# Performance work log

Measured on AMD Instinct MI355X. Metric: run time of the kernel, lower is better.

## Reference

```python
import jax, jax.numpy as jnp
import numpy as np

EMBED_DIM = 1024
NUM_HEADS = 16
HEAD_DIM = EMBED_DIM // NUM_HEADS
SCALE = HEAD_DIM ** -0.5


def setup_inputs() -> dict:
    key = jax.random.key(0)
    ks = jax.random.split(key, 12)
    B, S, D = 4, 2048, EMBED_DIM
    x = jax.random.normal(ks[0], (B, S, D), dtype=jnp.float32)
    key_padding_mask = jax.random.randint(ks[1], (B, S), 0, 2).astype(jnp.bool_)
    init = 1.0 / np.sqrt(D)
    def lin(kw, kb):
        W = jax.random.uniform(kw, (D, D), minval=-init, maxval=init, dtype=jnp.float32)
        b = jax.random.uniform(kb, (D,), minval=-init, maxval=init, dtype=jnp.float32)
        return W, b
    Wq, bq = lin(ks[2], ks[3])
    Wk, bk = lin(ks[4], ks[5])
    Wv, bv = lin(ks[6], ks[7])
    Wo, bo = lin(ks[8], ks[9])
    return {"x": x, "key_padding_mask": key_padding_mask,
            "Wq": Wq, "bq": bq, "Wk": Wk, "bk": bk,
            "Wv": Wv, "bv": bv, "Wo": Wo, "bo": bo}


def reference(x, key_padding_mask, Wq, bq, Wk, bk, Wv, bv, Wo, bo):
    B, S, D = x.shape
    H, Hd = NUM_HEADS, HEAD_DIM
    # projections (torch Linear: y = x @ W.T + b)
    q = (x @ Wq.T + bq).reshape(B, S, H, Hd).transpose(0, 2, 1, 3)  # [B,H,S,Hd]
    k = (x @ Wk.T + bk).reshape(B, S, H, Hd).transpose(0, 2, 1, 3)
    v = (x @ Wv.T + bv).reshape(B, S, H, Hd).transpose(0, 2, 1, 3)
    scores = jnp.einsum('bhqd,bhkd->bhqk', q, k) * SCALE  # [B,H,S,S]
    mask = key_padding_mask[:, None, None, :]  # [B,1,1,S]
    scores = jnp.where(mask, -jnp.inf, scores)
    probs = jax.nn.softmax(scores, axis=-1)
    # dropout p=0.0 (inference) -> identity
    out = jnp.einsum('bhqk,bhkd->bhqd', probs, v)  # [B,H,S,Hd]
    out = out.transpose(0, 2, 1, 3).reshape(B, S, D)
    return out @ Wo.T + bo
```

## Files before the change

### kernel.cpp

```cpp
#include <hip/hip_runtime.h>
#include <stdint.h>

typedef __bf16 bf16;
typedef __bf16 bf16x8 __attribute__((ext_vector_type(8)));
typedef float f32x4 __attribute__((ext_vector_type(4)));

#define SEQ 2048
#define NHEAD 16
#define HDIM 64
#define DMODEL 1024
#define NBATCH 4
#define ATT_SCALE 0.18033688011112042f
#define SEQHD (SEQ * HDIM)
#define BHSTRIDE (2 * SEQHD)


__device__ __forceinline__ void gload_lds16(const bf16* g, bf16* l) {
  __builtin_amdgcn_global_load_lds(
      (const __attribute__((address_space(1))) uint32_t*)g,
      (__attribute__((address_space(3))) uint32_t*)l, 16, 0, 0);
}

__device__ __forceinline__ uint32_t pk2(float a, float b) {
  bf16 x = (bf16)a, y = (bf16)b;
  return (uint32_t)__builtin_bit_cast(uint16_t, x) |
         ((uint32_t)__builtin_bit_cast(uint16_t, y) << 16);
}

__global__ __launch_bounds__(256) void cvt_kernel(const float* __restrict__ src,
                                                  bf16* __restrict__ dst) {
  size_t i = ((size_t)blockIdx.x * 256 + threadIdx.x) * 16;
#pragma unroll
  for (int j = 0; j < 2; ++j) {
    float4 f0 = *(const float4*)(src + i + j * 8);
    float4 f1 = *(const float4*)(src + i + j * 8 + 4);
    bf16x8 v;
    v[0] = (bf16)f0.x; v[1] = (bf16)f0.y; v[2] = (bf16)f0.z; v[3] = (bf16)f0.w;
    v[4] = (bf16)f1.x; v[5] = (bf16)f1.y; v[6] = (bf16)f1.z; v[7] = (bf16)f1.w;
    *(bf16x8*)(dst + i + j * 8) = v;
  }
}

__global__ __launch_bounds__(256) void prep_kernel(
    const float* __restrict__ Wq, const float* __restrict__ Wk,
    const float* __restrict__ Wv, bf16* __restrict__ Wbf3,
    int* __restrict__ posv, int* __restrict__ inv) {
  __shared__ int sums[256];
  const int bx = blockIdx.x, t = threadIdx.x;
  if (bx < 768) {
    const float* s = bx < 256 ? Wq : (bx < 512 ? Wk : Wv);
    bf16* d = Wbf3 + (size_t)(bx >> 8) * DMODEL * DMODEL;
    size_t i = ((size_t)(bx & 255) * 256 + t) * 16;
#pragma unroll
    for (int j = 0; j < 2; ++j) {
      float4 f0 = *(const float4*)(s + i + j * 8);
      float4 f1 = *(const float4*)(s + i + j * 8 + 4);
      bf16x8 v;
      v[0] = (bf16)f0.x; v[1] = (bf16)f0.y; v[2] = (bf16)f0.z; v[3] = (bf16)f0.w;
      v[4] = (bf16)f1.x; v[5] = (bf16)f1.y; v[6] = (bf16)f1.z; v[7] = (bf16)f1.w;
      *(bf16x8*)(d + i + j * 8) = v;
    }
    return;
  }
  const int b = bx - 768;
  int* m = posv + b * SEQ;
  int* iv = inv + b * SEQ;
  int f[8], cnt = 0;
#pragma unroll
  for (int j = 0; j < 8; ++j) {
    int x = m[t * 8 + j];
    int unm = (x < 0) ? 0 : ((x & 0x40000000) ? 1 : (x == 0 ? 1 : 0));
    f[j] = unm; cnt += unm;
    iv[t * 8 + j] = 0;
  }
  sums[t] = cnt;
  __syncthreads();
  if (t == 0) {
    int acc = 0;
#pragma unroll 8
    for (int i = 0; i < 256; ++i) { int s = sums[i]; sums[i] = acc; acc += s; }
  }
  __syncthreads();
  int p = sums[t];
#pragma unroll
  for (int j = 0; j < 8; ++j) {
    m[t * 8 + j] = (int)((f[j] ? 0x40000000u : 0x80000000u) | (unsigned)p);
    if (f[j]) iv[p] = t * 8 + j;
    p += f[j];
  }
}

__global__ __launch_bounds__(256) void mega_kernel(
    const bf16* __restrict__ xb, const bf16* __restrict__ Wall,
    const float* __restrict__ bq, const float* __restrict__ bk,
    const float* __restrict__ bv, const int* __restrict__ posv,
    const int* __restrict__ inv, bf16* __restrict__ Qall,
    bf16* __restrict__ kv, const float* __restrict__ Wo,
    bf16* __restrict__ Wobf) {
  __shared__ __align__(16) bf16 lW[64 * 64];
  __shared__ __align__(16) bf16 lXw[4][32 * 64];
  const int bx = blockIdx.x;
  const int t = threadIdx.x, wave = t >> 6, lane = t & 63;
  const int quad = lane >> 4, c = lane & 15;
  const int sr = lane >> 3, sg = lane & 7;
  const int swzc = (sg ^ sr) * 8;

  if (bx >= 2048) {
    size_t i = ((size_t)(bx - 2048) * 256 + t) * 16;
#pragma unroll
    for (int j = 0; j < 2; ++j) {
      float4 f0 = *(const float4*)(Wo + i + j * 8);
      float4 f1 = *(const float4*)(Wo + i + j * 8 + 4);
      bf16x8 v;
      v[0] = (bf16)f0.x; v[1] = (bf16)f0.y; v[2] = (bf16)f0.z; v[3] = (bf16)f0.w;
      v[4] = (bf16)f1.x; v[5] = (bf16)f1.y; v[6] = (bf16)f1.z; v[7] = (bf16)f1.w;
      *(bf16x8*)(Wobf + i + j * 8) = v;
    }
    return;
  }

  if (bx < 1024) {
    const int m0 = (bx & 63) * 128;
    const int h = bx >> 6;
    const bf16* W = Wall + (size_t)(h * HDIM) * DMODEL;
    bf16* pw = lXw[wave];
    const bf16* aS = xb + (size_t)(m0 + wave * 32 + sr) * DMODEL + swzc;
    const bf16* wS = W + (size_t)(wave * 8 + sr) * DMODEL + swzc;
    f32x4 acc[2][4] = {};
    for (int k0 = 0; k0 < DMODEL; k0 += 64) {
      __syncthreads();
      gload_lds16(wS + k0, lW + wave * 512);
      gload_lds16(wS + 32 * DMODEL + k0, lW + wave * 512 + 2048);
#pragma unroll
      for (int ii = 0; ii < 4; ++ii)
        gload_lds16(aS + k0 + (size_t)ii * 8 * DMODEL, pw + ii * 512);
      __syncthreads();
#pragma unroll
      for (int kk = 0; kk < 2; ++kk) {
        bf16x8 af[2], bfr[4];
#pragma unroll
        for (int mi = 0; mi < 2; ++mi) {
          int row = mi * 16 + c;
          af[mi] = *(const bf16x8*)(pw + row * 64 + (((kk * 4 + quad) ^ (row & 7)) * 8));
        }
#pragma unroll
        for (int ni = 0; ni < 4; ++ni) {
          int row = ni * 16 + c;
          bfr[ni] = *(const bf16x8*)(lW + row * 64 + (((kk * 4 + quad) ^ (row & 7)) * 8));
        }
#pragma unroll
        for (int mi = 0; mi < 2; ++mi)
#pragma unroll
          for (int ni = 0; ni < 4; ++ni)
            acc[mi][ni] = __builtin_amdgcn_mfma_f32_16x16x32_bf16(af[mi], bfr[ni], acc[mi][ni], 0, 0, 0);
      }
    }
#pragma unroll
    for (int ni = 0; ni < 4; ++ni) {
      int hd = ni * 16 + c;
      float bqv = bq[h * HDIM + hd];
#pragma unroll
      for (int mi = 0; mi < 2; ++mi)
#pragma unroll
        for (int r = 0; r < 4; ++r) {
          int tok = m0 + wave * 32 + mi * 16 + quad * 4 + r;
          int b = tok >> 11, s = tok & 2047;
          Qall[((size_t)(b * NHEAD + h) * SEQ + s) * HDIM + hd] =
              (bf16)((acc[mi][ni][r] + bqv) * ATT_SCALE);
        }
    }
    return;
  }

  const int idx = bx - 1024;
  const int xi = idx & 31, yi = idx >> 5;
  const int b_loc = xi >> 4, mb = xi & 15;
  const int isV = yi >> 4, h = yi & 15;
  int v2 = posv[b_loc * SEQ + SEQ - 1];
  int nk = (v2 & 0x3FFFFFFF) + (v2 >= 0 ? 1 : 0);
  const int c0 = mb * 128;
  if (c0 >= nk) return;
  const bf16* W = Wall + (size_t)(1 + isV) * DMODEL * DMODEL + (size_t)(h * HDIM) * DMODEL;
  const float* bias = (isV ? bv : bk) + h * HDIM;
  bf16* pw = lXw[wave];
  const bf16* wS = W + (size_t)(wave * 8 + sr) * DMODEL + swzc;
  const int* invb = inv + b_loc * SEQ;
  int grow[4];
#pragma unroll
  for (int ii = 0; ii < 4; ++ii)
    grow[ii] = invb[c0 + wave * 32 + ii * 8 + sr];
  const bf16* xbb = xb + (size_t)b_loc * SEQ * DMODEL + swzc;
  f32x4 acc[2][4] = {};
  for (int k0 = 0; k0 < DMODEL; k0 += 64) {
    __syncthreads();
    gload_lds16(wS + k0, lW + wave * 512);
    gload_lds16(wS + 32 * DMODEL + k0, lW + wave * 512 + 2048);
#pragma unroll
    for (int ii = 0; ii < 4; ++ii)
      gload_lds16(xbb + (size_t)grow[ii] * DMODEL + k0, pw + ii * 512);
    __syncthreads();
#pragma unroll
    for (int kk = 0; kk < 2; ++kk) {
      bf16x8 af[2], bfr[4];
#pragma unroll
      for (int mi = 0; mi < 2; ++mi) {
        int row = mi * 16 + c;
        af[mi] = *(const bf16x8*)(pw + row * 64 + (((kk * 4 + quad) ^ (row & 7)) * 8));
      }
#pragma unroll
      for (int ni = 0; ni < 4; ++ni) {
        int row = ni * 16 + c;
        bfr[ni] = *(const bf16x8*)(lW + row * 64 + (((kk * 4 + quad) ^ (row & 7)) * 8));
      }
#pragma unroll
      for (int mi = 0; mi < 2; ++mi)
#pragma unroll
        for (int ni = 0; ni < 4; ++ni)
          acc[mi][ni] = __builtin_amdgcn_mfma_f32_16x16x32_bf16(af[mi], bfr[ni], acc[mi][ni], 0, 0, 0);
    }
  }
  bf16* base = kv + (size_t)(b_loc * NHEAD + h) * BHSTRIDE;
#pragma unroll
  for (int ni = 0; ni < 4; ++ni) {
    int hd = ni * 16 + c;
    float bv_ = bias[hd];
#pragma unroll
    for (int mi = 0; mi < 2; ++mi)
#pragma unroll
      for (int r = 0; r < 4; ++r) {
        int dst = c0 + wave * 32 + mi * 16 + quad * 4 + r;
        float val = (dst < nk) ? (acc[mi][ni][r] + bv_) : 0.0f;
        if (isV) base[SEQHD + (size_t)hd * SEQ + dst] = (bf16)val;
        else     base[(size_t)dst * HDIM + hd] = (bf16)val;
      }
  }
}

__global__ __launch_bounds__(256) void kvproj_kernel(
    const bf16* __restrict__ xb, const bf16* __restrict__ Wall,
    const float* __restrict__ bk, const float* __restrict__ bv,
    const int* __restrict__ posv, const int* __restrict__ inv,
    bf16* __restrict__ kv) {
  __shared__ __align__(16) bf16 lW[64 * 64];
  __shared__ __align__(16) bf16 lXw[4][32 * 64];
  const int t = threadIdx.x, wave = t >> 6, lane = t & 63;
  const int quad = lane >> 4, c = lane & 15;
  const int bx = blockIdx.x;
  const int b_loc = bx >> 4, mb = bx & 15;
  const int nt = blockIdx.y;
  const int isV = nt >> 4, h = nt & 15;
  int v2 = posv[b_loc * SEQ + SEQ - 1];
  int nk = (v2 & 0x3FFFFFFF) + (v2 >= 0 ? 1 : 0);
  const int c0 = mb * 128;
  if (c0 >= nk) return;
  const bf16* W = Wall + (size_t)(1 + isV) * DMODEL * DMODEL + (size_t)(h * HDIM) * DMODEL;
  const float* bias = (isV ? bv : bk) + h * HDIM;
  bf16* pw = lXw[wave];
  const int sr = lane >> 3, sg = lane & 7;
  const int swzc = (sg ^ sr) * 8;
  const bf16* wS = W + (size_t)(wave * 8 + sr) * DMODEL + swzc;
  const int* invb = inv + b_loc * SEQ;
  int grow[4];
#pragma unroll
  for (int ii = 0; ii < 4; ++ii)
    grow[ii] = invb[c0 + wave * 32 + ii * 8 + sr];
  const bf16* xbb = xb + (size_t)b_loc * SEQ * DMODEL + swzc;
  f32x4 acc[2][4] = {};
  for (int k0 = 0; k0 < DMODEL; k0 += 64) {
    __syncthreads();
    gload_lds16(wS + k0, lW + wave * 512);
    gload_lds16(wS + 32 * DMODEL + k0, lW + wave * 512 + 2048);
#pragma unroll
    for (int ii = 0; ii < 4; ++ii)
      gload_lds16(xbb + (size_t)grow[ii] * DMODEL + k0, pw + ii * 512);
    __syncthreads();
#pragma unroll
    for (int kk = 0; kk < 2; ++kk) {
      bf16x8 af[2], bfr[4];
#pragma unroll
      for (int mi = 0; mi < 2; ++mi) {
        int row = mi * 16 + c;
        af[mi] = *(const bf16x8*)(pw + row * 64 + (((kk * 4 + quad) ^ (row & 7)) * 8));
      }
#pragma unroll
      for (int ni = 0; ni < 4; ++ni) {
        int row = ni * 16 + c;
        bfr[ni] = *(const bf16x8*)(lW + row * 64 + (((kk * 4 + quad) ^ (row & 7)) * 8));
      }
#pragma unroll
      for (int mi = 0; mi < 2; ++mi)
#pragma unroll
        for (int ni = 0; ni < 4; ++ni)
          acc[mi][ni] = __builtin_amdgcn_mfma_f32_16x16x32_bf16(af[mi], bfr[ni], acc[mi][ni], 0, 0, 0);
    }
  }
  bf16* base = kv + (size_t)(b_loc * NHEAD + h) * BHSTRIDE;
#pragma unroll
  for (int ni = 0; ni < 4; ++ni) {
    int hd = ni * 16 + c;
    float bv_ = bias[hd];
#pragma unroll
    for (int mi = 0; mi < 2; ++mi)
#pragma unroll
      for (int r = 0; r < 4; ++r) {
        int dst = c0 + wave * 32 + mi * 16 + quad * 4 + r;
        float val = (dst < nk) ? (acc[mi][ni][r] + bv_) : 0.0f;
        if (isV) base[SEQHD + (size_t)hd * SEQ + dst] = (bf16)val;
        else     base[(size_t)dst * HDIM + hd] = (bf16)val;
      }
  }
}

__global__ __launch_bounds__(256, 4) void attn4_kernel(
    const bf16* __restrict__ Qall, const bf16* __restrict__ KV,
    const int* __restrict__ posv, bf16* __restrict__ O, int chunk) {
  __shared__ __align__(16) bf16 lK[2][64 * 64];
  __shared__ __align__(16) bf16 lV[2][64 * 64];
  __shared__ __align__(16) bf16 lPw[4][16 * 64];
  const int t = threadIdx.x, wave = t >> 6, lane = t & 63;
  const int quad = lane >> 4, c = lane & 15;
  const int i = blockIdx.x;
  const int xcd = i & 7, slot = i >> 3;
  const int bhl = xcd * 4 + (slot >> 5);
  const int qt = slot & 31;
  const int b_loc = bhl >> 4, h = bhl & 15;
  const int b = chunk * 2 + b_loc;
  const int q0 = qt * 64 + wave * 16;
  const bf16* Qh = Qall + (size_t)(b * NHEAD + h) * SEQHD;
  const bf16* Kb = KV + (size_t)(b_loc * NHEAD + h) * BHSTRIDE;
  const bf16* Vtb = Kb + SEQHD;
  bf16* pw = lPw[wave];

  int v2 = posv[b * SEQ + SEQ - 1];
  int nk = (v2 & 0x3FFFFFFF) + (v2 >= 0 ? 1 : 0);
  int NT = ((nk + 63) >> 6) << 6;

  const int srow = t >> 3;
  const int sswz = (t & 7) ^ (srow & 7);
  const bf16* kSrc = Kb + (size_t)srow * HDIM + sswz * 8;
  const bf16* vSrc = Vtb + (size_t)srow * SEQ + sswz * 8;
  const int sOff = wave * 512;

  bf16x8 qf[2];
#pragma unroll
  for (int kk = 0; kk < 2; ++kk)
    qf[kk] = *(const bf16x8*)(Qh + (size_t)(q0 + c) * HDIM + kk * 32 + quad * 8);

  f32x4 oacc[4] = {};
  float mrun = -1e30f, lrun = 0.0f;

  const int pbase = c * 64 + (quad & 1) * 4;
  const int pswz = c & 7;

#pragma unroll
  for (int i2 = 0; i2 < 2; ++i2) {
    gload_lds16(kSrc + i2 * 32 * HDIM, &lK[0][0] + sOff + i2 * 2048);
    gload_lds16(vSrc + (size_t)i2 * 32 * SEQ, &lV[0][0] + sOff + i2 * 2048);
  }
  __syncthreads();

  int idx = 0;
  for (int kt = 0; kt < NT; kt += 64, idx ^= 1) {
    if (kt + 64 < NT) {
      const bf16* ks = kSrc + (size_t)(kt + 64) * HDIM;
      const bf16* vs = vSrc + (kt + 64);
      bf16* kD = &lK[0][0] + (idx ^ 1) * 4096 + sOff;
      bf16* vD = &lV[0][0] + (idx ^ 1) * 4096 + sOff;
#pragma unroll
      for (int i2 = 0; i2 < 2; ++i2) {
        gload_lds16(ks + i2 * 32 * HDIM, kD + i2 * 2048);
        gload_lds16(vs + (size_t)i2 * 32 * SEQ, vD + i2 * 2048);
      }
    }
    const bf16* lKc = &lK[0][0] + idx * 4096;
    const bf16* lVc = &lV[0][0] + idx * 4096;

    f32x4 sacc[4] = {};
    __builtin_amdgcn_s_setprio(1);
#pragma unroll
    for (int kk = 0; kk < 2; ++kk) {
      bf16x8 kf[4];
#pragma unroll
      for (int ni = 0; ni < 4; ++ni) {
        int row = ni * 16 + c;
        kf[ni] = *(const bf16x8*)(lKc + row * 64 + (((kk * 4 + quad) ^ (row & 7)) * 8));
      }
#pragma unroll
      for (int ni = 0; ni < 4; ++ni)
        sacc[ni] = __builtin_amdgcn_mfma_f32_16x16x32_bf16(kf[ni], qf[kk], sacc[ni], 0, 0, 0);
    }
    __builtin_amdgcn_s_setprio(0);

    if (kt + 64 > nk) {
      int base = kt + quad * 4 - nk;
#pragma unroll
      for (int ni = 0; ni < 4; ++ni)
#pragma unroll
        for (int r = 0; r < 4; ++r)
          if (base + ni * 16 + r >= 0) sacc[ni][r] = -3e38f;
    }

    float m1 = fmaxf(fmaxf(sacc[0][0], sacc[0][1]), sacc[0][2]);
    float m2 = fmaxf(fmaxf(sacc[0][3], sacc[1][0]), sacc[1][1]);
    float m3 = fmaxf(fmaxf(sacc[1][2], sacc[1][3]), sacc[2][0]);
    float m4 = fmaxf(fmaxf(sacc[2][1], sacc[2][2]), sacc[2][3]);
    float m5 = fmaxf(fmaxf(sacc[3][0], sacc[3][1]), sacc[3][2]);
    float mx = fmaxf(fmaxf(fmaxf(m1, m2), m3), fmaxf(fmaxf(m4, m5), sacc[3][3]));
    mx = fmaxf(mx, __shfl_xor(mx, 16));
    mx = fmaxf(mx, __shfl_xor(mx, 32));

    if (!__all(mx - mrun <= 8.0f)) {
      float mn = fmaxf(mrun, mx);
      float al = __builtin_amdgcn_exp2f(mrun - mn);
      mrun = mn;
      lrun *= al;
      float al4[4];
#pragma unroll
      for (int r = 0; r < 4; ++r) al4[r] = __shfl(al, quad * 4 + r);
#pragma unroll
      for (int ni = 0; ni < 4; ++ni)
#pragma unroll
        for (int r = 0; r < 4; ++r) oacc[ni][r] *= al4[r];
    }

    float rs = 0.0f;
#pragma unroll
    for (int ni = 0; ni < 4; ++ni)
#pragma unroll
      for (int r = 0; r < 4; ++r) {
        float e = __builtin_amdgcn_exp2f(sacc[ni][r] - mrun);
        sacc[ni][r] = e; rs += e;
      }
    rs += __shfl_xor(rs, 16);
    rs += __shfl_xor(rs, 32);
    lrun += rs;

#pragma unroll
    for (int ni = 0; ni < 4; ++ni) {
      uint2 u;
      u.x = pk2(sacc[ni][0], sacc[ni][1]);
      u.y = pk2(sacc[ni][2], sacc[ni][3]);
      int sl = pbase + (((ni * 2 + (quad >> 1)) ^ pswz) * 8);
      *(uint2*)(pw + sl) = u;
    }

    __builtin_amdgcn_s_setprio(1);
#pragma unroll
    for (int kk = 0; kk < 2; ++kk) {
      bf16x8 pf, vfr[4];
      pf = *(const bf16x8*)(pw + c * 64 + (((kk * 4 + quad) ^ (c & 7)) * 8));
#pragma unroll
      for (int ni = 0; ni < 4; ++ni) {
        int row = ni * 16 + c;
        vfr[ni] = *(const bf16x8*)(lVc + row * 64 + (((kk * 4 + quad) ^ (row & 7)) * 8));
      }
#pragma unroll
      for (int ni = 0; ni < 4; ++ni)
        oacc[ni] = __builtin_amdgcn_mfma_f32_16x16x32_bf16(pf, vfr[ni], oacc[ni], 0, 0, 0);
    }
    __builtin_amdgcn_s_setprio(0);

    __syncthreads();
  }

  float linv = lrun > 0.0f ? 1.0f / lrun : 0.0f;
  float linv4[4];
#pragma unroll
  for (int r = 0; r < 4; ++r) linv4[r] = __shfl(linv, quad * 4 + r);
#pragma unroll
  for (int r = 0; r < 4; ++r) {
    size_t tok = (size_t)b * SEQ + q0 + quad * 4 + r;
#pragma unroll
    for (int ni = 0; ni < 4; ++ni)
      O[tok * DMODEL + h * HDIM + ni * 16 + c] = (bf16)(oacc[ni][r] * linv4[r]);
  }
}

__global__ __launch_bounds__(256) void outproj_kernel(
    const bf16* __restrict__ O, const bf16* __restrict__ Wob,
    const float* __restrict__ bo, float* __restrict__ out) {
  __shared__ __align__(16) bf16 lW[64 * 64];
  __shared__ __align__(16) bf16 lXw[4][32 * 64];
  const int t = threadIdx.x, wave = t >> 6, lane = t & 63;
  const int quad = lane >> 4, c = lane & 15;
  const int m0 = blockIdx.x * 128;
  const int n0 = blockIdx.y * 64;
  bf16* pw = lXw[wave];
  const int sr = lane >> 3, sg = lane & 7;
  const bf16* aS = O + (size_t)(m0 + wave * 32 + sr) * DMODEL + ((sg ^ sr) * 8);
  const bf16* wS = Wob + (size_t)(n0 + wave * 8 + sr) * DMODEL + ((sg ^ sr) * 8);
  f32x4 acc[2][4] = {};
  for (int k0 = 0; k0 < DMODEL; k0 += 64) {
    __syncthreads();
    gload_lds16(wS + k0, lW + wave * 512);
    gload_lds16(wS + 32 * DMODEL + k0, lW + wave * 512 + 2048);
#pragma unroll
    for (int ii = 0; ii < 4; ++ii)
      gload_lds16(aS + k0 + (size_t)ii * 8 * DMODEL, pw + ii * 512);
    __syncthreads();
#pragma unroll
    for (int kk = 0; kk < 2; ++kk) {
      bf16x8 af[2], bfr[4];
#pragma unroll
      for (int mi = 0; mi < 2; ++mi) {
        int row = mi * 16 + c;
        af[mi] = *(const bf16x8*)(pw + row * 64 + (((kk * 4 + quad) ^ (row & 7)) * 8));
      }
#pragma unroll
      for (int ni = 0; ni < 4; ++ni) {
        int row = ni * 16 + c;
        bfr[ni] = *(const bf16x8*)(lW + row * 64 + (((kk * 4 + quad) ^ (row & 7)) * 8));
      }
#pragma unroll
      for (int mi = 0; mi < 2; ++mi)
#pragma unroll
        for (int ni = 0; ni < 4; ++ni)
          acc[mi][ni] = __builtin_amdgcn_mfma_f32_16x16x32_bf16(af[mi], bfr[ni], acc[mi][ni], 0, 0, 0);
    }
  }
#pragma unroll
  for (int ni = 0; ni < 4; ++ni) {
    int gn = n0 + ni * 16 + c;
    float bv_ = bo[gn];
#pragma unroll
    for (int mi = 0; mi < 2; ++mi)
#pragma unroll
      for (int r = 0; r < 4; ++r) {
        int gm = m0 + wave * 32 + mi * 16 + quad * 4 + r;
        out[(size_t)gm * DMODEL + gn] = acc[mi][ni][r] + bv_;
      }
  }
}

extern "C" void kernel_launch(void* const* d_in, const int* in_sizes, int n_in,
                              void* d_out, int out_size, void* d_ws, size_t ws_size,
                              hipStream_t stream) {
  const float* x  = (const float*)d_in[0];
  int*         posv = (int*)d_in[1];
  const float* Wq = (const float*)d_in[2]; const float* bq = (const float*)d_in[3];
  const float* Wk = (const float*)d_in[4]; const float* bk = (const float*)d_in[5];
  const float* Wv = (const float*)d_in[6]; const float* bv = (const float*)d_in[7];
  const float* Wo = (const float*)d_in[8]; const float* bo = (const float*)d_in[9];
  float* out = (float*)d_out;
  char* outc = (char*)d_out;
  char* xc   = (char*)d_in[0];
  const size_t half = (size_t)NBATCH * SEQ * DMODEL * 2;
  const size_t qtr  = half / 2;

  bf16* Qall = (bf16*)d_out;
  bf16* xbf  = (bf16*)(outc + half);
  bf16* KV   = (bf16*)xc;
  bf16* O    = (bf16*)(xc + half);
  bf16* Wbf3 = (bf16*)(xc + half + qtr);
  int*  inv  = (int*)(xc + half + qtr + (size_t)3 * DMODEL * DMODEL * 2);
  bf16* Wobf = (bf16*)d_in[2];

  cvt_kernel<<<dim3(2048), 256, 0, stream>>>(x, xbf);
  prep_kernel<<<dim3(772), 256, 0, stream>>>(Wq, Wk, Wv, Wbf3, posv, inv);
  mega_kernel<<<dim3(2304), 256, 0, stream>>>(xbf, Wbf3, bq, bk, bv, posv, inv,
                                              Qall, KV, Wo, Wobf);
  attn4_kernel<<<dim3(1024), 256, 0, stream>>>(Qall, KV, posv, O, 0);
  kvproj_kernel<<<dim3(32, 32), 256, 0, stream>>>(xbf + (size_t)2 * SEQ * DMODEL, Wbf3, bk, bv,
                                                  posv + 2 * SEQ, inv + 2 * SEQ, KV);
  attn4_kernel<<<dim3(1024), 256, 0, stream>>>(Qall, KV, posv, O, 1);
  outproj_kernel<<<dim3(64, 16), 256, 0, stream>>>(O, Wobf, bo, out);
}
```

Measured before the change: 274.9 us.

## Double-buffer LDS tiles in projection GEMMs to overlap loads with MFMA

Doubles the LDS staging buffers in the Q/K/V projection paths and the output projection, and restructures the K loop so the next 64-wide K slice is issued via global_load_lds while the current slice is consumed by MFMAs. This halves the barriers per K step and aims to hide global-memory latency behind compute. LDS use per block doubles (32KB), which may lower occupancy. The correctness of the direct-to-LDS async loads relies on the barrier draining outstanding loads.

New measurement: 305.6 us. 1.11x slower.

```diff
diff --git a/kernel.cpp b/kernel.cpp
--- a/kernel.cpp
+++ b/kernel.cpp
@@ -97,8 +97,8 @@
     const int* __restrict__ inv, bf16* __restrict__ Qall,
     bf16* __restrict__ kv, const float* __restrict__ Wo,
     bf16* __restrict__ Wobf) {
-  __shared__ __align__(16) bf16 lW[64 * 64];
-  __shared__ __align__(16) bf16 lXw[4][32 * 64];
+  __shared__ __align__(16) bf16 lW[2][64 * 64];
+  __shared__ __align__(16) bf16 lXw[2][4][32 * 64];
   const int bx = blockIdx.x;
   const int t = threadIdx.x, wave = t >> 6, lane = t & 63;
   const int quad = lane >> 4, c = lane & 15;
@@ -123,30 +123,30 @@
     const int m0 = (bx & 63) * 128;
     const int h = bx >> 6;
     const bf16* W = Wall + (size_t)(h * HDIM) * DMODEL;
-    bf16* pw = lXw[wave];
     const bf16* aS = xb + (size_t)(m0 + wave * 32 + sr) * DMODEL + swzc;
     const bf16* wS = W + (size_t)(wave * 8 + sr) * DMODEL + swzc;
     f32x4 acc[2][4] = {};
-    for (int k0 = 0; k0 < DMODEL; k0 += 64) {
-      __syncthreads();
-      gload_lds16(wS + k0, lW + wave * 512);
-      gload_lds16(wS + 32 * DMODEL + k0, lW + wave * 512 + 2048);
+
+    auto stage = [&](int k0, bf16* lWd, bf16* pwd) {
+      gload_lds16(wS + k0, lWd + wave * 512);
+      gload_lds16(wS + 32 * DMODEL + k0, lWd + wave * 512 + 2048);
 #pragma unroll
       for (int ii = 0; ii < 4; ++ii)
-        gload_lds16(aS + k0 + (size_t)ii * 8 * DMODEL, pw + ii * 512);
-      __syncthreads();
+        gload_lds16(aS + k0 + (size_t)ii * 8 * DMODEL, pwd + ii * 512);
+    };
+    auto compute = [&](const bf16* lWc, const bf16* pwc) {
 #pragma unroll
       for (int kk = 0; kk < 2; ++kk) {
         bf16x8 af[2], bfr[4];
 #pragma unroll
         for (int mi = 0; mi < 2; ++mi) {
           int row = mi * 16 + c;
-          af[mi] = *(const bf16x8*)(pw + row * 64 + (((kk * 4 + quad) ^ (row & 7)) * 8));
+          af[mi] = *(const bf16x8*)(pwc + row * 64 + (((kk * 4 + quad) ^ (row & 7)) * 8));
         }
 #pragma unroll
         for (int ni = 0; ni < 4; ++ni) {
           int row = ni * 16 + c;
-          bfr[ni] = *(const bf16x8*)(lW + row * 64 + (((kk * 4 + quad) ^ (row & 7)) * 8));
+          bfr[ni] = *(const bf16x8*)(lWc + row * 64 + (((kk * 4 + quad) ^ (row & 7)) * 8));
         }
 #pragma unroll
         for (int mi = 0; mi < 2; ++mi)
@@ -154,6 +154,17 @@
           for (int ni = 0; ni < 4; ++ni)
             acc[mi][ni] = __builtin_amdgcn_mfma_f32_16x16x32_bf16(af[mi], bfr[ni], acc[mi][ni], 0, 0, 0);
       }
+    };
+
+    stage(0, lW[0], lXw[0][wave]);
+    __syncthreads();
+    for (int k0 = 0; k0 < DMODEL; k0 += 128) {
+      stage(k0 + 64, lW[1], lXw[1][wave]);
+      compute(lW[0], lXw[0][wave]);
+      __syncthreads();
+      if (k0 + 128 < DMODEL) stage(k0 + 128, lW[0], lXw[0][wave]);
+      compute(lW[1], lXw[1][wave]);
+      __syncthreads();
     }
 #pragma unroll
     for (int ni = 0; ni < 4; ++ni) {
@@ -182,7 +193,6 @@
   if (c0 >= nk) return;
   const bf16* W = Wall + (size_t)(1 + isV) * DMODEL * DMODEL + (size_t)(h * HDIM) * DMODEL;
   const float* bias = (isV ? bv : bk) + h * HDIM;
-  bf16* pw = lXw[wave];
   const bf16* wS = W + (size_t)(wave * 8 + sr) * DMODEL + swzc;
   const int* invb = inv + b_loc * SEQ;
   int grow[4];
@@ -191,26 +201,27 @@
     grow[ii] = invb[c0 + wave * 32 + ii * 8 + sr];
   const bf16* xbb = xb + (size_t)b_loc * SEQ * DMODEL + swzc;
   f32x4 acc[2][4] = {};
-  for (int k0 = 0; k0 < DMODEL; k0 += 64) {
-    __syncthreads();
-    gload_lds16(wS + k0, lW + wave * 512);
-    gload_lds16(wS + 32 * DMODEL + k0, lW + wave * 512 + 2048);
+
+  auto stage = [&](int k0, bf16* lWd, bf16* pwd) {
+    gload_lds16(wS + k0, lWd + wave * 512);
+    gload_lds16(wS + 32 * DMODEL + k0, lWd + wave * 512 + 2048);
 #pragma unroll
     for (int ii = 0; ii < 4; ++ii)
-      gload_lds16(xbb + (size_t)grow[ii] * DMODEL + k0, pw + ii * 512);
-    __syncthreads();
+      gload_lds16(xbb + (size_t)grow[ii] * DMODEL + k0, pwd + ii * 512);
+  };
+  auto compute = [&](const bf16* lWc, const bf16* pwc) {
 #pragma unroll
     for (int kk = 0; kk < 2; ++kk) {
       bf16x8 af[2], bfr[4];
 #pragma unroll
       for (int mi = 0; mi < 2; ++mi) {
         int row = mi * 16 + c;
-        af[mi] = *(const bf16x8*)(pw + row * 64 + (((kk * 4 + quad) ^ (row & 7)) * 8));
+        af[mi] = *(const bf16x8*)(pwc + row * 64 + (((kk * 4 + quad) ^ (row & 7)) * 8));
       }
 #pragma unroll
       for (int ni = 0; ni < 4; ++ni) {
         int row = ni * 16 + c;
-        bfr[ni] = *(const bf16x8*)(lW + row * 64 + (((kk * 4 + quad) ^ (row & 7)) * 8));
+        bfr[ni] = *(const bf16x8*)(lWc + row * 64 + (((kk * 4 + quad) ^ (row & 7)) * 8));
       }
 #pragma unroll
       for (int mi = 0; mi < 2; ++mi)
@@ -218,6 +229,17 @@
         for (int ni = 0; ni < 4; ++ni)
           acc[mi][ni] = __builtin_amdgcn_mfma_f32_16x16x32_bf16(af[mi], bfr[ni], acc[mi][ni], 0, 0, 0);
     }
+  };
+
+  stage(0, lW[0], lXw[0][wave]);
+  __syncthreads();
+  for (int k0 = 0; k0 < DMODEL; k0 += 128) {
+    stage(k0 + 64, lW[1], lXw[1][wave]);
+    compute(lW[0], lXw[0][wave]);
+    __syncthreads();
+    if (k0 + 128 < DMODEL) stage(k0 + 128, lW[0], lXw[0][wave]);
+    compute(lW[1], lXw[1][wave]);
+    __syncthreads();
   }
   bf16* base = kv + (size_t)(b_loc * NHEAD + h) * BHSTRIDE;
 #pragma unroll
@@ -241,8 +263,8 @@
     const float* __restrict__ bk, const float* __restrict__ bv,
     const int* __restrict__ posv, const int* __restrict__ inv,
     bf16* __restrict__ kv) {
-  __shared__ __align__(16) bf16 lW[64 * 64];
-  __shared__ __align__(16) bf16 lXw[4][32 * 64];
+  __shared__ __align__(16) bf16 lW[2][64 * 64];
+  __shared__ __align__(16) bf16 lXw[2][4][32 * 64];
   const int t = threadIdx.x, wave = t >> 6, lane = t & 63;
   const int quad = lane >> 4, c = lane & 15;
   const int bx = blockIdx.x;
@@ -255,7 +277,6 @@
   if (c0 >= nk) return;
   const bf16* W = Wall + (size_t)(1 + isV) * DMODEL * DMODEL + (size_t)(h * HDIM) * DMODEL;
   const float* bias = (isV ? bv : bk) + h * HDIM;
-  bf16* pw = lXw[wave];
   const int sr = lane >> 3, sg = lane & 7;
   const int swzc = (sg ^ sr) * 8;
   const bf16* wS = W + (size_t)(wave * 8 + sr) * DMODEL + swzc;
@@ -266,26 +287,27 @@
     grow[ii] = invb[c0 + wave * 32 + ii * 8 + sr];
   const bf16* xbb = xb + (size_t)b_loc * SEQ * DMODEL + swzc;
   f32x4 acc[2][4] = {};
-  for (int k0 = 0; k0 < DMODEL; k0 += 64) {
-    __syncthreads();
-    gload_lds16(wS + k0, lW + wave * 512);
-    gload_lds16(wS + 32 * DMODEL + k0, lW + wave * 512 + 2048);
+
+  auto stage = [&](int k0, bf16* lWd, bf16* pwd) {
+    gload_lds16(wS + k0, lWd + wave * 512);
+    gload_lds16(wS + 32 * DMODEL + k0, lWd + wave * 512 + 2048);
 #pragma unroll
     for (int ii = 0; ii < 4; ++ii)
-      gload_lds16(xbb + (size_t)grow[ii] * DMODEL + k0, pw + ii * 512);
-    __syncthreads();
+      gload_lds16(xbb + (size_t)grow[ii] * DMODEL + k0, pwd + ii * 512);
+  };
+  auto compute = [&](const bf16* lWc, const bf16* pwc) {
 #pragma unroll
     for (int kk = 0; kk < 2; ++kk) {
       bf16x8 af[2], bfr[4];
 #pragma unroll
       for (int mi = 0; mi < 2; ++mi) {
         int row = mi * 16 + c;
-        af[mi] = *(const bf16x8*)(pw + row * 64 + (((kk * 4 + quad) ^ (row & 7)) * 8));
+        af[mi] = *(const bf16x8*)(pwc + row * 64 + (((kk * 4 + quad) ^ (row & 7)) * 8));
       }
 #pragma unroll
       for (int ni = 0; ni < 4; ++ni) {
         int row = ni * 16 + c;
-        bfr[ni] = *(const bf16x8*)(lW + row * 64 + (((kk * 4 + quad) ^ (row & 7)) * 8));
+        bfr[ni] = *(const bf16x8*)(lWc + row * 64 + (((kk * 4 + quad) ^ (row & 7)) * 8));
       }
 #pragma unroll
       for (int mi = 0; mi < 2; ++mi)
@@ -293,6 +315,17 @@
         for (int ni = 0; ni < 4; ++ni)
           acc[mi][ni] = __builtin_amdgcn_mfma_f32_16x16x32_bf16(af[mi], bfr[ni], acc[mi][ni], 0, 0, 0);
     }
+  };
+
+  stage(0, lW[0], lXw[0][wave]);
+  __syncthreads();
+  for (int k0 = 0; k0 < DMODEL; k0 += 128) {
+    stage(k0 + 64, lW[1], lXw[1][wave]);
+    compute(lW[0], lXw[0][wave]);
+    __syncthreads();
+    if (k0 + 128 < DMODEL) stage(k0 + 128, lW[0], lXw[0][wave]);
+    compute(lW[1], lXw[1][wave]);
+    __syncthreads();
   }
   bf16* base = kv + (size_t)(b_loc * NHEAD + h) * BHSTRIDE;
 #pragma unroll
@@ -479,37 +512,37 @@
 __global__ __launch_bounds__(256) void outproj_kernel(
     const bf16* __restrict__ O, const bf16* __restrict__ Wob,
     const float* __restrict__ bo, float* __restrict__ out) {
-  __shared__ __align__(16) bf16 lW[64 * 64];
-  __shared__ __align__(16) bf16 lXw[4][32 * 64];
+  __shared__ __align__(16) bf16 lW[2][64 * 64];
+  __shared__ __align__(16) bf16 lXw[2][4][32 * 64];
   const int t = threadIdx.x, wave = t >> 6, lane = t & 63;
   const int quad = lane >> 4, c = lane & 15;
   const int m0 = blockIdx.x * 128;
   const int n0 = blockIdx.y * 64;
-  bf16* pw = lXw[wave];
   const int sr = lane >> 3, sg = lane & 7;
   const bf16* aS = O + (size_t)(m0 + wave * 32 + sr) * DMODEL + ((sg ^ sr) * 8);
   const bf16* wS = Wob + (size_t)(n0 + wave * 8 + sr) * DMODEL + ((sg ^ sr) * 8);
   f32x4 acc[2][4] = {};
-  for (int k0 = 0; k0 < DMODEL; k0 += 64) {
-    __syncthreads();
-    gload_lds16(wS + k0, lW + wave * 512);
-    gload_lds16(wS + 32 * DMODEL + k0, lW + wave * 512 + 2048);
+
+  auto stage = [&](int k0, bf16* lWd, bf16* pwd) {
+    gload_lds16(wS + k0, lWd + wave * 512);
+    gload_lds16(wS + 32 * DMODEL + k0, lWd + wave * 512 + 2048);
 #pragma unroll
     for (int ii = 0; ii < 4; ++ii)
-      gload_lds16(aS + k0 + (size_t)ii * 8 * DMODEL, pw + ii * 512);
-    __syncthreads();
+      gload_lds16(aS + k0 + (size_t)ii * 8 * DMODEL, pwd + ii * 512);
+  };
+  auto compute = [&](const bf16* lWc, const bf16* pwc) {
 #pragma unroll
     for (int kk = 0; kk < 2; ++kk) {
       bf16x8 af[2], bfr[4];
 #pragma unroll
       for (int mi = 0; mi < 2; ++mi) {
         int row = mi * 16 + c;
-        af[mi] = *(const bf16x8*)(pw + row * 64 + (((kk * 4 + quad) ^ (row & 7)) * 8));
+        af[mi] = *(const bf16x8*)(pwc + row * 64 + (((kk * 4 + quad) ^ (row & 7)) * 8));
       }
 #pragma unroll
       for (int ni = 0; ni < 4; ++ni) {
         int row = ni * 16 + c;
-        bfr[ni] = *(const bf16x8*)(lW + row * 64 + (((kk * 4 + quad) ^ (row & 7)) * 8));
+        bfr[ni] = *(const bf16x8*)(lWc + row * 64 + (((kk * 4 + quad) ^ (row & 7)) * 8));
       }
 #pragma unroll
       for (int mi = 0; mi < 2; ++mi)
@@ -517,6 +550,17 @@
         for (int ni = 0; ni < 4; ++ni)
           acc[mi][ni] = __builtin_amdgcn_mfma_f32_16x16x32_bf16(af[mi], bfr[ni], acc[mi][ni], 0, 0, 0);
     }
+  };
+
+  stage(0, lW[0], lXw[0][wave]);
+  __syncthreads();
+  for (int k0 = 0; k0 < DMODEL; k0 += 128) {
+    stage(k0 + 64, lW[1], lXw[1][wave]);
+    compute(lW[0], lXw[0][wave]);
+    __syncthreads();
+    if (k0 + 128 < DMODEL) stage(k0 + 128, lW[0], lXw[0][wave]);
+    compute(lW[1], lXw[1][wave]);
+    __syncthreads();
   }
 #pragma unroll
   for (int ni = 0; ni < 4; ++ni) {
```
